# Performance work log

Measured on AMD Instinct MI355X. Metric: run time of the kernel, lower is better.

The kernel has to match this reference:

```python
import jax, jax.numpy as jnp
import numpy as np

N_COLS = 4096
N_ROWS = 4096
H = 64          # args.hidden1
S = 2           # per-edge supp feature count (cv_supp/vc_supp dim 0)
S_VO = 2        # vo_supp feature dim
S_CO = 2        # co_supp feature dim
EDGE_DENSITY = 0.03


def setup_inputs() -> dict:
    key = jax.random.key(0)
    ks = jax.random.split(key, 20)
    col_hidden = jax.random.normal(ks[0], (N_COLS, H), jnp.float32)
    row_hidden = jax.random.normal(ks[1], (N_ROWS, H), jnp.float32)
    obj_hidden = jax.random.normal(ks[2], (1, H), jnp.float32)
    # sparse bipartite adjacency encoded in supp[0] != 0 (as in the TF code)
    mask = jax.random.bernoulli(ks[3], EDGE_DENSITY, (N_ROWS, N_COLS))
    cv_supp = jax.random.normal(ks[4], (S, N_ROWS, N_COLS), jnp.float32) * mask[None]
    vc_supp = jnp.transpose(cv_supp, (0, 2, 1))  # [S, ncols, nrows]
    vo_supp = jax.random.normal(ks[5], (N_COLS, S_VO), jnp.float32)
    co_supp = jax.random.normal(ks[6], (N_ROWS, S_CO), jnp.float32)
    w = 0.05
    W_vo = jax.random.normal(ks[7], (2 * H, H), jnp.float32) * w
    W_oc = jax.random.normal(ks[8], (2 * H, H), jnp.float32) * w
    W_vc = jax.random.normal(ks[9], (2 * H, H), jnp.float32) * w
    W_co = jax.random.normal(ks[10], (2 * H, H), jnp.float32) * w
    W_ov = jax.random.normal(ks[11], (2 * H, H), jnp.float32) * w
    W_cv = jax.random.normal(ks[12], (2 * H, H), jnp.float32) * w
    # attention scorer nets: Dense(concat_dim -> 1) + sigmoid
    w_attn_vo = jax.random.normal(ks[13], (2 * H + S_VO, 1), jnp.float32) * 0.1
    b_attn_vo = jnp.zeros((), jnp.float32)
    w_attn_co = jax.random.normal(ks[14], (2 * H + S_CO, 1), jnp.float32) * 0.1
    b_attn_co = jnp.zeros((), jnp.float32)
    # pairwise attn nets decomposed into [col | supp | row] weight slices
    w_cv_col = jax.random.normal(ks[15], (H,), jnp.float32) * 0.1
    w_cv_supp = jax.random.normal(ks[16], (S,), jnp.float32) * 0.1
    w_cv_row = jax.random.normal(ks[17], (H,), jnp.float32) * 0.1
    b_cv = jnp.zeros((), jnp.float32)
    w_vc_row = jax.random.normal(ks[18], (H,), jnp.float32) * 0.1
    w_vc_supp = jax.random.normal(ks[19], (S,), jnp.float32) * 0.1
    w_vc_col = jax.random.normal(jax.random.fold_in(key, 99), (H,), jnp.float32) * 0.1
    b_vc = jnp.zeros((), jnp.float32)
    return dict(col_hidden=col_hidden, row_hidden=row_hidden, obj_hidden=obj_hidden,
                cv_supp=cv_supp, vc_supp=vc_supp, vo_supp=vo_supp, co_supp=co_supp,
                W_vo=W_vo, W_oc=W_oc, W_vc=W_vc, W_co=W_co, W_ov=W_ov, W_cv=W_cv,
                w_attn_vo=w_attn_vo, b_attn_vo=b_attn_vo,
                w_attn_co=w_attn_co, b_attn_co=b_attn_co,
                w_cv_col=w_cv_col, w_cv_supp=w_cv_supp, w_cv_row=w_cv_row, b_cv=b_cv,
                w_vc_row=w_vc_row, w_vc_supp=w_vc_supp, w_vc_col=w_vc_col, b_vc=b_vc)


def _forward(col_hidden, row_hidden, obj_hidden, cv_supp, vc_supp, vo_supp, co_supp,
             W_vo, W_oc, W_vc, W_co, W_ov, W_cv,
             w_attn_vo, b_attn_vo, w_attn_co, b_attn_co,
             w_cv_col, w_cv_supp, w_cv_row, b_cv,
             w_vc_row, w_vc_supp, w_vc_col, b_vc):
    act = jax.nn.relu
    ncols, nrows = col_hidden.shape[0], row_hidden.shape[0]
    # ---- v -> o: attend over all columns, update obj node ----
    vo_in = jnp.concatenate([col_hidden, vo_supp,
                             jnp.broadcast_to(obj_hidden, (ncols, H))], axis=1)
    a_vo = jax.nn.sigmoid(vo_in @ w_attn_vo + b_attn_vo)          # [ncols, 1]
    v_o_out = a_vo.T @ col_hidden                                  # [1, H]
    obj = act(jnp.concatenate([obj_hidden, v_o_out], axis=1) @ W_vo)
    # ---- v -> c: per-row ragged neighbor attention, vectorized via masked pairwise scores ----
    nbr_cv = cv_supp[0] != 0                                       # [nrows, ncols]
    logits_cv = ((row_hidden @ w_cv_row)[:, None]
                 + (col_hidden @ w_cv_col)[None, :]
                 + jnp.einsum('snc,s->nc', cv_supp, w_cv_supp) + b_cv)
    score_cv = jnp.where(nbr_cv, jax.nn.sigmoid(logits_cv), 0.0)   # [nrows, ncols]
    v_out = score_cv @ col_hidden                                  # [nrows, H]
    o_c_out = act(jnp.concatenate([jnp.broadcast_to(obj, (nrows, H)), row_hidden], axis=1) @ W_oc)
    row_next = act(jnp.concatenate([o_c_out, v_out], axis=1) @ W_vc)
    # ---- c -> o ----
    co_in = jnp.concatenate([row_next, co_supp,
                             jnp.broadcast_to(obj, (nrows, H))], axis=1)
    a_co = jax.nn.sigmoid(co_in @ w_attn_co + b_attn_co)           # [nrows, 1]
    c_o_out = a_co.T @ row_next                                    # [1, H]
    obj = act(jnp.concatenate([obj, c_o_out], axis=1) @ W_co)
    # ---- c -> v ----
    nbr_vc = vc_supp[0] != 0                                       # [ncols, nrows]
    logits_vc = ((col_hidden @ w_vc_col)[:, None]
                 + (row_next @ w_vc_row)[None, :]
                 + jnp.einsum('scn,s->cn', vc_supp, w_vc_supp) + b_vc)
    score_vc = jnp.where(nbr_vc, jax.nn.sigmoid(logits_vc), 0.0)   # [ncols, nrows]
    c_out = score_vc @ row_next                                    # [ncols, H]
    o_v_out = act(jnp.concatenate([jnp.broadcast_to(obj, (ncols, H)), col_hidden], axis=1) @ W_ov)
    col_next = act(jnp.concatenate([o_v_out, c_out], axis=1) @ W_cv)
    return col_next, row_next, obj


def reference(col_hidden, row_hidden, obj_hidden, cv_supp, vc_supp, vo_supp, co_supp,
              W_vo, W_oc, W_vc, W_co, W_ov, W_cv,
              w_attn_vo, b_attn_vo, w_attn_co, b_attn_co,
              w_cv_col, w_cv_supp, w_cv_row, b_cv,
              w_vc_row, w_vc_supp, w_vc_col, b_vc):
    col_next, row_next, obj = _forward(
        col_hidden, row_hidden, obj_hidden, cv_supp, vc_supp, vo_supp, co_supp,
        W_vo, W_oc, W_vc, W_co, W_ov, W_cv,
        w_attn_vo, b_attn_vo, w_attn_co, b_attn_co,
        w_cv_col, w_cv_supp, w_cv_row, b_cv,
        w_vc_row, w_vc_supp, w_vc_col, b_vc)
    # original layer also passes the supp tensors through unchanged
    return (col_next, row_next, obj, cv_supp, vc_supp, vo_supp, co_supp)
```

## Files before the change

### kernel.cpp

```cpp
#include <hip/hip_runtime.h>
#include <math.h>

typedef float f4 __attribute__((ext_vector_type(4)));

#define PLANE (4096*4096)

#define OUT_COL 0
#define OUT_ROW 262144
#define OUT_OBJ 524288
#define OUT_CV  524352
#define OUT_VC  34078784
#define OUT_VO  67633216
#define OUT_CO  67641408

#define WS_VO_P 0
#define WS_CO_P 4096
#define WS_OBJ1 8192
#define WS_RDCV 8256
#define WS_CDCV 12352
#define WS_RDVC 16448
#define WS_CDVC 20544
#define WS_PART 24640

__device__ __forceinline__ float sigf(float x) {
    return 1.0f / (1.0f + __expf(-x));
}

__device__ __forceinline__ float enc_sj(float s, int j) {
    return __uint_as_float((__float_as_uint(s) & 0xFFFFF000u) | (unsigned)j);
}

__device__ __forceinline__ void attn_body64(
    int blk, int t, const float* __restrict__ X, const float* __restrict__ supp,
    const float* __restrict__ obj, const float* __restrict__ wat,
    const float* __restrict__ bat, float* __restrict__ accP,
    const float* __restrict__ wextra, float* __restrict__ dextra,
    float* sA, float* sAcc)
{
    const int w = t >> 6, lane = t & 63;
    if (t < 64) {
        const int i = blk * 64 + t;
        float od = 0.f;
        for (int h = 0; h < 64; ++h) od += obj[h] * wat[66 + h];
        float x = bat[0] + od + supp[i*2] * wat[64] + supp[i*2+1] * wat[65];
        const f4* Xr = (const f4*)(X + i*64);
        f4 xd = 0.f, dd = 0.f;
        #pragma unroll
        for (int q = 0; q < 16; ++q) {
            f4 xv = Xr[q];
            xd += xv * ((const f4*)wat)[q];
            if (wextra) dd += xv * ((const f4*)wextra)[q];
        }
        x += xd.x + xd.y + xd.z + xd.w;
        if (dextra) dextra[i] = dd.x + dd.y + dd.z + dd.w;
        sA[t] = sigf(x);
        sAcc[t] = 0.f;
    }
    __syncthreads();
    float partial = 0.f;
    const int jbase = blk * 64 + w * 16;
    for (int j = 0; j < 16; ++j)
        partial += sA[w*16 + j] * X[(jbase + j)*64 + lane];
    atomicAdd(&sAcc[lane], partial);
    __syncthreads();
    if (t < 64) accP[blk*64 + t] = sAcc[t];
}

__global__ __launch_bounds__(256) void k_front(
    const float* __restrict__ col_hidden, const float* __restrict__ row_hidden,
    const float* __restrict__ w_cv_col, const float* __restrict__ w_vc_col,
    const float* __restrict__ w_cv_row,
    float* __restrict__ cdcv, float* __restrict__ cdvc, float* __restrict__ rdcv,
    const float* __restrict__ vo_supp, const float* __restrict__ co_supp,
    float* __restrict__ out_vo, float* __restrict__ out_co,
    const float* __restrict__ obj_hidden, const float* __restrict__ w_attn_vo,
    const float* __restrict__ b_attn_vo, float* __restrict__ voP)
{
    __shared__ float sA[64];
    __shared__ float sAcc[64];
    const int t = threadIdx.x;
    if (blockIdx.x < 3072) {
        const int gw = blockIdx.x * 4 + (t >> 6);
        const int lane = t & 63;
        const int which = gw >> 12;
        const int row = gw & 4095;
        const float* x; const float* w; float* dst;
        if (which == 0)      { x = col_hidden; w = w_cv_col; dst = cdcv; }
        else if (which == 1) { x = col_hidden; w = w_vc_col; dst = cdvc; }
        else                 { x = row_hidden; w = w_cv_row; dst = rdcv; }
        float v = x[row * 64 + lane] * w[lane];
        #pragma unroll
        for (int off = 32; off; off >>= 1) v += __shfl_down(v, off, 64);
        if (lane == 0) dst[row] = v;
        return;
    }
    if (blockIdx.x < 3088) {
        const int idx = (blockIdx.x - 3072) * 256 + t;
        if (idx < 2048) ((f4*)out_vo)[idx] = ((const f4*)vo_supp)[idx];
        else            ((f4*)out_co)[idx - 2048] = ((const f4*)co_supp)[idx - 2048];
        return;
    }
    attn_body64(blockIdx.x - 3088, t, col_hidden, vo_supp, obj_hidden,
                w_attn_vo, b_attn_vo, voP, nullptr, nullptr, sA, sAcc);
}

__global__ __launch_bounds__(256) void k_attn(
    const float* __restrict__ X, const float* __restrict__ supp,
    const float* __restrict__ obj, const float* __restrict__ wat,
    const float* __restrict__ bat, float* __restrict__ accP,
    const float* __restrict__ wextra, float* __restrict__ dextra)
{
    __shared__ float sA[64];
    __shared__ float sAcc[64];
    attn_body64(blockIdx.x, threadIdx.x, X, supp, obj, wat, bat, accP,
                wextra, dextra, sA, sAcc);
}

__global__ __launch_bounds__(256, 4) void k_big(
    const float* __restrict__ supp0, const float* __restrict__ supp1,
    const float* __restrict__ Bm,
    const float* __restrict__ rdot, const float* __restrict__ cdot,
    const float* __restrict__ wsup, const float* __restrict__ bias,
    float* __restrict__ vout, float* __restrict__ pass0, float* __restrict__ pass1,
    const float* __restrict__ objL, const float* __restrict__ objRp,
    const float* __restrict__ Wobj, float* __restrict__ objDst)
{
    __shared__ __align__(16) float list[4][256];
    const int t = threadIdx.x;

    if (blockIdx.x == 1024) {
        float* red = &list[0][0];
        if (t < 64) {
            float r = 0.f;
            for (int b = 0; b < 64; ++b) r += objRp[b*64 + t];
            red[t] = r;
        }
        __syncthreads();
        if (t < 64) {
            float acc = 0.f;
            for (int k = 0; k < 64; ++k) acc += objL[k] * Wobj[k*64 + t];
            for (int k = 0; k < 64; ++k) acc += red[k] * Wobj[(64+k)*64 + t];
            objDst[t] = fmaxf(acc, 0.f);
        }
        return;
    }

    const int w = t >> 6, lane = t & 63;
    const int r = blockIdx.x * 4 + w;
    const float w0 = wsup[0], w1 = wsup[1], bv = bias[0];
    const float rd = rdot[r];
    float* Lrow = &list[w][0];

    int base = 0;
    #pragma unroll 2
    for (int c = 0; c < 16; ++c) {
        const size_t g = (size_t)r * 4096 + c * 256 + lane * 4;
        f4 a0 = *(const f4*)(supp0 + g);
        f4 a1 = *(const f4*)(supp1 + g);
        __builtin_nontemporal_store(a0, (f4*)(pass0 + g));
        __builtin_nontemporal_store(a1, (f4*)(pass1 + g));
        const f4 cd = *(const f4*)(cdot + c * 256 + lane * 4);
        f4 lg = rd + cd + w0 * a0 + w1 * a1 + bv;
        const int c0 = (a0.x != 0.f), c1 = (a0.y != 0.f);
        const int c2 = (a0.z != 0.f), c3 = (a0.w != 0.f);
        const int m = c0 + c1 + c2 + c3;
        int sum = m;
        #pragma unroll
        for (int d = 1; d < 64; d <<= 1) {
            int x = __shfl_up(sum, d, 64);
            if (lane >= d) sum += x;
        }
        int pos = base + sum - m;
        const int jb = c * 256 + lane * 4;
        if (c0) { if (pos < 256) Lrow[pos] = enc_sj(sigf(lg.x), jb + 0); ++pos; }
        if (c1) { if (pos < 256) Lrow[pos] = enc_sj(sigf(lg.y), jb + 1); ++pos; }
        if (c2) { if (pos < 256) Lrow[pos] = enc_sj(sigf(lg.z), jb + 2); ++pos; }
        if (c3) { if (pos < 256) Lrow[pos] = enc_sj(sigf(lg.w), jb + 3); ++pos; }
        base += __shfl(sum, 63, 64);
    }
    asm volatile("s_waitcnt lgkmcnt(0)" ::: "memory");
    __builtin_amdgcn_sched_barrier(0);

    const int n = base < 256 ? base : 256;
    float acc = 0.f;
    #pragma unroll 4
    for (int k = 0; k < n; ++k) {
        const unsigned u = __float_as_uint(Lrow[k]);
        const int j = (int)(u & 0xFFFu);
        const float s = __uint_as_float(u & 0xFFFFF000u);
        acc += s * Bm[(size_t)j * 64 + lane];
    }
    vout[(size_t)r * 64 + lane] = acc;
}

__global__ __launch_bounds__(256) void k_mlp2(
    const float* __restrict__ objx, const float* __restrict__ base,
    const float* __restrict__ W1, const float* __restrict__ part,
    const float* __restrict__ W2, float* __restrict__ dst)
{
    __shared__ float mid[4][64];
    __shared__ float accs[4][64];
    const int t = threadIdx.x, w = t >> 6, h = t & 63;
    const int n = blockIdx.x * 4 + w;
    accs[w][h] = part[(size_t)n * 64 + h];
    float m = 0.f;
    for (int k = 0; k < 64; ++k) m += objx[k] * W1[k*64 + h];
    for (int k = 0; k < 64; ++k) m += base[n*64 + k] * W1[(64+k)*64 + h];
    mid[w][h] = fmaxf(m, 0.f);
    __syncthreads();
    float o = 0.f;
    for (int k = 0; k < 64; ++k) o += mid[w][k] * W2[k*64 + h];
    for (int k = 0; k < 64; ++k) o += accs[w][k] * W2[(64+k)*64 + h];
    dst[n*64 + h] = fmaxf(o, 0.f);
}

extern "C" void kernel_launch(void* const* d_in, const int* in_sizes, int n_in,
                              void* d_out, int out_size, void* d_ws, size_t ws_size,
                              hipStream_t stream)
{
    const float* col_hidden = (const float*)d_in[0];
    const float* row_hidden = (const float*)d_in[1];
    const float* obj_hidden = (const float*)d_in[2];
    const float* cv_supp    = (const float*)d_in[3];
    const float* vc_supp    = (const float*)d_in[4];
    const float* vo_supp    = (const float*)d_in[5];
    const float* co_supp    = (const float*)d_in[6];
    const float* W_vo       = (const float*)d_in[7];
    const float* W_oc       = (const float*)d_in[8];
    const float* W_vc       = (const float*)d_in[9];
    const float* W_co       = (const float*)d_in[10];
    const float* W_ov       = (const float*)d_in[11];
    const float* W_cv       = (const float*)d_in[12];
    const float* w_attn_vo  = (const float*)d_in[13];
    const float* b_attn_vo  = (const float*)d_in[14];
    const float* w_attn_co  = (const float*)d_in[15];
    const float* b_attn_co  = (const float*)d_in[16];
    const float* w_cv_col   = (const float*)d_in[17];
    const float* w_cv_supp  = (const float*)d_in[18];
    const float* w_cv_row   = (const float*)d_in[19];
    const float* b_cv       = (const float*)d_in[20];
    const float* w_vc_row   = (const float*)d_in[21];
    const float* w_vc_supp  = (const float*)d_in[22];
    const float* w_vc_col   = (const float*)d_in[23];
    const float* b_vc       = (const float*)d_in[24];

    float* out = (float*)d_out;
    float* ws  = (float*)d_ws;

    k_front<<<3152, 256, 0, stream>>>(col_hidden, row_hidden, w_cv_col, w_vc_col, w_cv_row,
                                      ws + WS_CDCV, ws + WS_CDVC, ws + WS_RDCV,
                                      vo_supp, co_supp, out + OUT_VO, out + OUT_CO,
                                      obj_hidden, w_attn_vo, b_attn_vo, ws + WS_VO_P);
    k_big<<<1025, 256, 0, stream>>>(cv_supp, cv_supp + PLANE, col_hidden,
                                    ws + WS_RDCV, ws + WS_CDCV, w_cv_supp, b_cv,
                                    ws + WS_PART, out + OUT_CV, out + OUT_CV + PLANE,
                                    obj_hidden, ws + WS_VO_P, W_vo, ws + WS_OBJ1);
    k_mlp2<<<1024, 256, 0, stream>>>(ws + WS_OBJ1, row_hidden, W_oc, ws + WS_PART, W_vc,
                                     out + OUT_ROW);
    k_attn<<<64, 256, 0, stream>>>(out + OUT_ROW, co_supp, ws + WS_OBJ1, w_attn_co, b_attn_co,
                                   ws + WS_CO_P, w_vc_row, ws + WS_RDVC);
    k_big<<<1025, 256, 0, stream>>>(vc_supp, vc_supp + PLANE, out + OUT_ROW,
                                    ws + WS_CDVC, ws + WS_RDVC, w_vc_supp, b_vc,
                                    ws + WS_PART, out + OUT_VC, out + OUT_VC + PLANE,
                                    ws + WS_OBJ1, ws + WS_CO_P, W_co, out + OUT_OBJ);
    k_mlp2<<<1024, 256, 0, stream>>>(out + OUT_OBJ, col_hidden, W_ov, ws + WS_PART, W_cv,
                                     out + OUT_COL);
}
```

Before: 567.3 us.

## Split passthrough copy into memcpy and use per-chunk LDS edge lists

Removes the fused nontemporal passthrough stores from the scoring kernel and copies each supp tensor to the output with hipMemcpyAsync. The scoring kernel then reads the supp values back from the output copy, which may hit in cache. The single 256-entry per-row edge list becomes 16 per-chunk lists of 31 entries plus a count, dropping the cross-chunk running base shuffle. This adds an extra read of the 128MB supp data per plane and caps edges per 256-column chunk at 31, which could drop edges on denser rows.

```diff
diff --git a/kernel.cpp b/kernel.cpp
--- a/kernel.cpp
+++ b/kernel.cpp
@@ -116,20 +116,20 @@
                 wextra, dextra, sA, sAcc);
 }
 
-__global__ __launch_bounds__(256, 4) void k_big(
-    const float* __restrict__ supp0, const float* __restrict__ supp1,
+__global__ __launch_bounds__(256, 4) void k_score(
+    const float* __restrict__ supp0c, const float* __restrict__ supp1c,
     const float* __restrict__ Bm,
     const float* __restrict__ rdot, const float* __restrict__ cdot,
     const float* __restrict__ wsup, const float* __restrict__ bias,
-    float* __restrict__ vout, float* __restrict__ pass0, float* __restrict__ pass1,
+    float* __restrict__ vout,
     const float* __restrict__ objL, const float* __restrict__ objRp,
     const float* __restrict__ Wobj, float* __restrict__ objDst)
 {
-    __shared__ __align__(16) float list[4][256];
+    __shared__ __align__(16) float list[4][16][32];
     const int t = threadIdx.x;
 
     if (blockIdx.x == 1024) {
-        float* red = &list[0][0];
+        float* red = &list[0][0][0];
         if (t < 64) {
             float r = 0.f;
             for (int b = 0; b < 64; ++b) r += objRp[b*64 + t];
@@ -149,16 +149,12 @@
     const int r = blockIdx.x * 4 + w;
     const float w0 = wsup[0], w1 = wsup[1], bv = bias[0];
     const float rd = rdot[r];
-    float* Lrow = &list[w][0];
-
-    int base = 0;
-    #pragma unroll 2
+
+    #pragma unroll 4
     for (int c = 0; c < 16; ++c) {
         const size_t g = (size_t)r * 4096 + c * 256 + lane * 4;
-        f4 a0 = *(const f4*)(supp0 + g);
-        f4 a1 = *(const f4*)(supp1 + g);
-        __builtin_nontemporal_store(a0, (f4*)(pass0 + g));
-        __builtin_nontemporal_store(a1, (f4*)(pass1 + g));
+        f4 a0 = *(const f4*)(supp0c + g);
+        f4 a1 = *(const f4*)(supp1c + g);
         const f4 cd = *(const f4*)(cdot + c * 256 + lane * 4);
         f4 lg = rd + cd + w0 * a0 + w1 * a1 + bv;
         const int c0 = (a0.x != 0.f), c1 = (a0.y != 0.f);
@@ -170,25 +166,28 @@
             int x = __shfl_up(sum, d, 64);
             if (lane >= d) sum += x;
         }
-        int pos = base + sum - m;
+        int pos = sum - m;
+        float* L = &list[w][c][0];
         const int jb = c * 256 + lane * 4;
-        if (c0) { if (pos < 256) Lrow[pos] = enc_sj(sigf(lg.x), jb + 0); ++pos; }
-        if (c1) { if (pos < 256) Lrow[pos] = enc_sj(sigf(lg.y), jb + 1); ++pos; }
-        if (c2) { if (pos < 256) Lrow[pos] = enc_sj(sigf(lg.z), jb + 2); ++pos; }
-        if (c3) { if (pos < 256) Lrow[pos] = enc_sj(sigf(lg.w), jb + 3); ++pos; }
-        base += __shfl(sum, 63, 64);
+        if (c0) { if (pos < 31) L[pos] = enc_sj(sigf(lg.x), jb + 0); ++pos; }
+        if (c1) { if (pos < 31) L[pos] = enc_sj(sigf(lg.y), jb + 1); ++pos; }
+        if (c2) { if (pos < 31) L[pos] = enc_sj(sigf(lg.z), jb + 2); ++pos; }
+        if (c3) { if (pos < 31) L[pos] = enc_sj(sigf(lg.w), jb + 3); ++pos; }
+        if (lane == 63) L[31] = __int_as_float(sum < 31 ? sum : 31);
     }
     asm volatile("s_waitcnt lgkmcnt(0)" ::: "memory");
     __builtin_amdgcn_sched_barrier(0);
 
-    const int n = base < 256 ? base : 256;
     float acc = 0.f;
-    #pragma unroll 4
-    for (int k = 0; k < n; ++k) {
-        const unsigned u = __float_as_uint(Lrow[k]);
-        const int j = (int)(u & 0xFFFu);
-        const float s = __uint_as_float(u & 0xFFFFF000u);
-        acc += s * Bm[(size_t)j * 64 + lane];
+    for (int c = 0; c < 16; ++c) {
+        const float* L = &list[w][c][0];
+        const int n = __float_as_int(L[31]);
+        for (int k = 0; k < n; ++k) {
+            const unsigned u = __float_as_uint(L[k]);
+            const int j = (int)(u & 0xFFFu);
+            const float s = __uint_as_float(u & 0xFFFFF000u);
+            acc += s * Bm[(size_t)j * 64 + lane];
+        }
     }
     vout[(size_t)r * 64 + lane] = acc;
 }
@@ -246,23 +245,26 @@
 
     float* out = (float*)d_out;
     float* ws  = (float*)d_ws;
+    const size_t SUPP_BYTES = (size_t)2 * PLANE * sizeof(float);
 
     k_front<<<3152, 256, 0, stream>>>(col_hidden, row_hidden, w_cv_col, w_vc_col, w_cv_row,
                                       ws + WS_CDCV, ws + WS_CDVC, ws + WS_RDCV,
                                       vo_supp, co_supp, out + OUT_VO, out + OUT_CO,
                                       obj_hidden, w_attn_vo, b_attn_vo, ws + WS_VO_P);
-    k_big<<<1025, 256, 0, stream>>>(cv_supp, cv_supp + PLANE, col_hidden,
-                                    ws + WS_RDCV, ws + WS_CDCV, w_cv_supp, b_cv,
-                                    ws + WS_PART, out + OUT_CV, out + OUT_CV + PLANE,
-                                    obj_hidden, ws + WS_VO_P, W_vo, ws + WS_OBJ1);
+    hipMemcpyAsync(out + OUT_CV, cv_supp, SUPP_BYTES, hipMemcpyDeviceToDevice, stream);
+    k_score<<<1025, 256, 0, stream>>>(out + OUT_CV, out + OUT_CV + PLANE, col_hidden,
+                                      ws + WS_RDCV, ws + WS_CDCV, w_cv_supp, b_cv,
+                                      ws + WS_PART,
+                                      obj_hidden, ws + WS_VO_P, W_vo, ws + WS_OBJ1);
     k_mlp2<<<1024, 256, 0, stream>>>(ws + WS_OBJ1, row_hidden, W_oc, ws + WS_PART, W_vc,
                                      out + OUT_ROW);
     k_attn<<<64, 256, 0, stream>>>(out + OUT_ROW, co_supp, ws + WS_OBJ1, w_attn_co, b_attn_co,
                                    ws + WS_CO_P, w_vc_row, ws + WS_RDVC);
-    k_big<<<1025, 256, 0, stream>>>(vc_supp, vc_supp + PLANE, out + OUT_ROW,
-                                    ws + WS_CDVC, ws + WS_RDVC, w_vc_supp, b_vc,
-                                    ws + WS_PART, out + OUT_VC, out + OUT_VC + PLANE,
-                                    ws + WS_OBJ1, ws + WS_CO_P, W_co, out + OUT_OBJ);
+    hipMemcpyAsync(out + OUT_VC, vc_supp, SUPP_BYTES, hipMemcpyDeviceToDevice, stream);
+    k_score<<<1025, 256, 0, stream>>>(out + OUT_VC, out + OUT_VC + PLANE, out + OUT_ROW,
+                                      ws + WS_CDVC, ws + WS_RDVC, w_vc_supp, b_vc,
+                                      ws + WS_PART,
+                                      ws + WS_OBJ1, ws + WS_CO_P, W_co, out + OUT_OBJ);
     k_mlp2<<<1024, 256, 0, stream>>>(out + OUT_OBJ, col_hidden, W_ov, ws + WS_PART, W_cv,
                                      out + OUT_COL);
 }
```

New measurement: 598.9 us. 1.06x slower.
